# Optimization experiments

Hardware: AMD Instinct MI355X
Metric: run time of the kernel (lower is better)

## Reference

```python
import jax, jax.numpy as jnp
import numpy as np

GROUP = 16
LORA_SCALE = 4.0  # lora_alpha(4*r)/r
EPS = 1e-5


def _dequant(q, scale):
    # q: [O, I] int codes in [0,15]; scale: [O, I//GROUP] per-group normalization
    O, I = q.shape
    s = jnp.repeat(scale, GROUP, axis=1)  # [O, I]
    return (q.astype(jnp.float32) / 15.0 * 2.0 - 1.0) * s


def setup_inputs() -> dict:
    key = jax.random.key(0)
    ks = jax.random.split(key, 6)
    B, D, L, R = 16384, 1024, 18, 32
    x = jax.random.normal(ks[0], (B, D), dtype=jnp.float32)
    q_weights = jax.random.randint(ks[1], (L, D, D), 0, 16, dtype=jnp.int32)
    scales = jax.random.uniform(ks[2], (L, D, D // GROUP), dtype=jnp.float32) * 0.05 + 0.005
    biases = jax.random.normal(ks[3], (L, D), dtype=jnp.float32) * 0.02
    lora_a = jax.random.normal(ks[4], (L, R, D), dtype=jnp.float32) * 0.02
    lora_b = jax.random.normal(ks[5], (L, D, R), dtype=jnp.float32) * 0.02
    ln_gamma = jnp.ones((5, D), dtype=jnp.float32)
    ln_beta = jnp.zeros((5, D), dtype=jnp.float32)
    return {"x": x, "q_weights": q_weights, "scales": scales, "biases": biases,
            "lora_a": lora_a, "lora_b": lora_b, "ln_gamma": ln_gamma, "ln_beta": ln_beta}


def _qlora_linear(x, q, scale, bias, la, lb):
    w = _dequant(q, scale)                       # [O, I]
    base = x @ w.T + bias                        # [B, O]
    lora = (x @ la.T) @ lb.T                     # [B, r] -> [B, O]
    return base + LORA_SCALE * lora


def _layernorm(x, g, b):
    mu = jnp.mean(x, axis=-1, keepdims=True)
    var = jnp.mean(jnp.square(x - mu), axis=-1, keepdims=True)
    return (x - mu) * jax.lax.rsqrt(var + EPS) * g + b


def reference(x, q_weights, scales, biases, lora_a, lora_b, ln_gamma, ln_beta):
    h = x
    for blk in range(6):
        r = h
        for j in range(3):
            li = 3 * blk + j
            r = _qlora_linear(r, q_weights[li], scales[li], biases[li], lora_a[li], lora_b[li])
            if j < 2:
                r = jax.nn.relu(r)
        h = r + h  # residual
        if blk < 5:
            h = _layernorm(h, ln_gamma[blk], ln_beta[blk])
    return h
```

## Files before the change

kernel.cpp:

```cpp
#include <hip/hip_runtime.h>
#include <cstdint>
#include <cstddef>

#define D 1024
#define BATCH 16384
#define NLAYERS 18
#define RR 32

typedef __attribute__((ext_vector_type(8))) __bf16 bf16x8;
typedef __attribute__((ext_vector_type(4))) float f32x4;
typedef __attribute__((address_space(3))) void lds_void_t;
typedef __attribute__((address_space(1))) void gmem_void_t;

union bfpack { unsigned short us[8]; int4 v; };

__device__ __forceinline__ unsigned short f2bf(float f) {
    unsigned int b = __builtin_bit_cast(unsigned int, f);
    b += 0x7fffu + ((b >> 16) & 1u);
    return (unsigned short)(b >> 16);
}
__device__ __forceinline__ float bf2f(unsigned short u) {
    return __builtin_bit_cast(float, (unsigned int)u << 16);
}

__global__ __launch_bounds__(256) void lora_dequant(
    const float* __restrict__ la, const float* __restrict__ lb,
    const int* __restrict__ q, const float* __restrict__ scales,
    unsigned short* __restrict__ weff) {
    __shared__ unsigned short lbs[64][40];
    __shared__ unsigned short lat[256][40];
    __shared__ unsigned short out_s[64][264];
    const int b = blockIdx.x;
    const int li = b >> 6;
    const int o0 = ((b >> 2) & 15) << 6;
    const int i0 = (b & 3) << 8;
    const int t = threadIdx.x;

    {
        const int row = t >> 2, qt = t & 3;
        const float* src = lb + ((size_t)(li * D) + o0 + row) * RR + qt * 8;
        float4 v0 = ((const float4*)src)[0], v1 = ((const float4*)src)[1];
        bfpack u;
        u.us[0] = f2bf(v0.x); u.us[1] = f2bf(v0.y); u.us[2] = f2bf(v0.z); u.us[3] = f2bf(v0.w);
        u.us[4] = f2bf(v1.x); u.us[5] = f2bf(v1.y); u.us[6] = f2bf(v1.z); u.us[7] = f2bf(v1.w);
        *(int4*)&lbs[row][qt * 8] = u.v;
    }
    {
        const int col = t;
#pragma unroll 8
        for (int r = 0; r < 32; ++r)
            lat[col][r] = f2bf(la[((size_t)li * RR + r) * D + i0 + col]);
    }
    __syncthreads();

    {
        const int wid = t >> 6, lane = t & 63;
        const int l15 = lane & 15, kgrp = lane >> 4;
        const int wrow = (wid >> 1) << 5;
        const int wcol = (wid & 1) << 7;
        bf16x8 a[2], bb[8];
#pragma unroll
        for (int f = 0; f < 2; ++f)
            a[f] = *(const bf16x8*)&lbs[wrow + (f << 4) + l15][kgrp << 3];
#pragma unroll
        for (int g = 0; g < 8; ++g)
            bb[g] = *(const bf16x8*)&lat[wcol + (g << 4) + l15][kgrp << 3];
        f32x4 acc[2][8];
#pragma unroll
        for (int i = 0; i < 2; ++i)
#pragma unroll
            for (int j = 0; j < 8; ++j) acc[i][j] = 0.0f;
#pragma unroll
        for (int mi = 0; mi < 2; ++mi)
#pragma unroll
            for (int ni = 0; ni < 8; ++ni)
                acc[mi][ni] = __builtin_amdgcn_mfma_f32_16x16x32_bf16(
                    a[mi], bb[ni], acc[mi][ni], 0, 0, 0);
#pragma unroll
        for (int mi = 0; mi < 2; ++mi) {
            const int row = wrow + (mi << 4) + (kgrp << 2);
#pragma unroll
            for (int ni = 0; ni < 8; ++ni) {
                const int col = wcol + (ni << 4) + l15;
#pragma unroll
                for (int r = 0; r < 4; ++r)
                    out_s[row + r][col] = f2bf(4.0f * acc[mi][ni][r]);
            }
        }
    }
    __syncthreads();

    const float c = 2.0f / 15.0f;
#pragma unroll 1
    for (int iter = 0; iter < 8; ++iter) {
        const int idx = (iter << 8) + t;
        const int row = idx >> 5, c8 = (idx & 31) << 3;
        const size_t grow = (size_t)li * D + o0 + row;
        const int col = i0 + c8;
        const float s = scales[grow * (D / 16) + (col >> 4)];
        const int* qp = q + grow * D + col;
        int4 q0 = ((const int4*)qp)[0], q1 = ((const int4*)qp)[1];
        bfpack lo;
        lo.v = *(const int4*)&out_s[row][c8];
        int qa[8] = {q0.x, q0.y, q0.z, q0.w, q1.x, q1.y, q1.z, q1.w};
        bfpack u;
#pragma unroll
        for (int j = 0; j < 8; ++j)
            u.us[j] = f2bf(((float)qa[j] * c - 1.0f) * s + bf2f(lo.us[j]));
        *(int4*)(weff + grow * D + col) = u.v;
    }
}

__global__ __launch_bounds__(256) void init_xb(const float* __restrict__ x,
                                               unsigned short* __restrict__ xb) {
    const size_t i = (size_t)blockIdx.x * 256 + threadIdx.x;
    float4 v = ((const float4*)x)[i];
    ushort4 u;
    u.x = f2bf(v.x); u.y = f2bf(v.y); u.z = f2bf(v.z); u.w = f2bf(v.w);
    ((ushort4*)xb)[i] = u;
}

#define SBAR() do { asm volatile("" ::: "memory"); __builtin_amdgcn_s_barrier(); asm volatile("" ::: "memory"); } while (0)

__global__ __launch_bounds__(512, 2) void gemm256(
    const unsigned short* __restrict__ xb, const unsigned short* __restrict__ w,
    const float* __restrict__ bias,
    unsigned short* __restrict__ outb, int mode) {
    __shared__ __align__(16) char smem[131072];
    const int tid = threadIdx.x;
    const int wid = tid >> 6, lane = tid & 63;
    const int bid = blockIdx.x + (blockIdx.y << 2);
    const int xcd = bid & 7, slot = bid >> 3;
    const int m0 = ((xcd << 3) + (slot >> 2)) << 8;
    const int n0 = (slot & 3) << 8;
    const int l15 = lane & 15, kgrp = lane >> 4;
    const int wrow = (wid >> 2) << 7;
    const int wcol = (wid & 3) << 6;

    f32x4 acc[8][4];
#pragma unroll
    for (int i = 0; i < 8; ++i)
#pragma unroll
        for (int j = 0; j < 4; ++j) acc[i][j] = 0.0f;

#define STAGE_HALF(hs, i_)                                                     \
    do {                                                                       \
        const int k0_ = (hs) << 5;                                             \
        char* sA_ = smem + ((hs) & 3) * 32768;                                 \
        const int off_ = (i_) * 8192 + (tid << 4);                             \
        const int r_ = off_ >> 6;                                              \
        const int j_ = ((off_ >> 4) & 3) ^ ((r_ >> 1) & 3);                    \
        const unsigned short* ga_ = xb + (size_t)(m0 + r_) * D + k0_ + (j_ << 3); \
        const unsigned short* gb_ = w + (size_t)(n0 + r_) * D + k0_ + (j_ << 3);  \
        char* lA_ = sA_ + (i_) * 8192 + (wid << 10);                           \
        __builtin_amdgcn_global_load_lds((const gmem_void_t*)ga_, (lds_void_t*)lA_, 16, 0, 0);          \
        __builtin_amdgcn_global_load_lds((const gmem_void_t*)gb_, (lds_void_t*)(lA_ + 16384), 16, 0, 0); \
    } while (0)

    STAGE_HALF(0, 0); STAGE_HALF(0, 1);
    STAGE_HALF(1, 0); STAGE_HALF(1, 1);
    STAGE_HALF(2, 0); STAGE_HALF(2, 1);
    asm volatile("s_waitcnt vmcnt(8)" ::: "memory");
    SBAR();

    for (int h = 0; h < 32; ++h) {
        const char* sA = smem + (h & 3) * 32768;
        const char* sB = sA + 16384;
        bf16x8 a[8], b[4];
#pragma unroll
        for (int f = 0; f < 4; ++f) {
            const int r = wrow + (f << 4) + l15;
            a[f] = *(const bf16x8*)(sA + (r << 6) + ((kgrp ^ ((r >> 1) & 3)) << 4));
        }
#pragma unroll
        for (int g = 0; g < 4; ++g) {
            const int r = wcol + (g << 4) + l15;
            b[g] = *(const bf16x8*)(sB + (r << 6) + ((kgrp ^ ((r >> 1) & 3)) << 4));
        }
        if (h < 29) STAGE_HALF(h + 3, 0);
        SBAR();
        asm volatile("s_waitcnt lgkmcnt(0)" ::: "memory");
        __builtin_amdgcn_s_setprio(1);
#pragma unroll
        for (int mi = 0; mi < 4; ++mi)
#pragma unroll
            for (int ni = 0; ni < 4; ++ni)
                acc[mi][ni] = __builtin_amdgcn_mfma_f32_16x16x32_bf16(
                    a[mi], b[ni], acc[mi][ni], 0, 0, 0);
        __builtin_amdgcn_s_setprio(0);
        SBAR();
#pragma unroll
        for (int f = 4; f < 8; ++f) {
            const int r = wrow + (f << 4) + l15;
            a[f] = *(const bf16x8*)(sA + (r << 6) + ((kgrp ^ ((r >> 1) & 3)) << 4));
        }
        if (h < 29) {
            STAGE_HALF(h + 3, 1);
            asm volatile("s_waitcnt vmcnt(8)" ::: "memory");
        } else if (h == 29) {
            asm volatile("s_waitcnt vmcnt(4)" ::: "memory");
        } else if (h == 30) {
            asm volatile("s_waitcnt vmcnt(0)" ::: "memory");
        }
        SBAR();
        asm volatile("s_waitcnt lgkmcnt(0)" ::: "memory");
        __builtin_amdgcn_s_setprio(1);
#pragma unroll
        for (int mi = 4; mi < 8; ++mi)
#pragma unroll
            for (int ni = 0; ni < 4; ++ni)
                acc[mi][ni] = __builtin_amdgcn_mfma_f32_16x16x32_bf16(
                    a[mi], b[ni], acc[mi][ni], 0, 0, 0);
        __builtin_amdgcn_s_setprio(0);
        SBAR();
    }

    const int crow = kgrp << 2;
    float bv[4];
#pragma unroll
    for (int ni = 0; ni < 4; ++ni) bv[ni] = bias[n0 + wcol + (ni << 4) + l15];
#pragma unroll
    for (int mi = 0; mi < 8; ++mi) {
        const int rbase = m0 + wrow + (mi << 4) + crow;
#pragma unroll
        for (int ni = 0; ni < 4; ++ni) {
            const int col = n0 + wcol + (ni << 4) + l15;
#pragma unroll
            for (int r = 0; r < 4; ++r) {
                float v = acc[mi][ni][r] + bv[ni];
                if (mode == 0) v = v > 0.0f ? v : 0.0f;
                outb[(size_t)(rbase + r) * D + col] = f2bf(v);
            }
        }
    }
}

__global__ __launch_bounds__(256) void resid_ln_b(
    unsigned short* __restrict__ hb, const unsigned short* __restrict__ vb,
    const float* __restrict__ gamma, const float* __restrict__ beta) {
    const int row = blockIdx.x;
    const int t = threadIdx.x;
    unsigned short* hr = hb + (size_t)row * D;
    ushort4 hv = ((const ushort4*)hr)[t];
    ushort4 vv = ((const ushort4*)(vb + (size_t)row * D))[t];
    float4 v;
    v.x = bf2f(hv.x) + bf2f(vv.x); v.y = bf2f(hv.y) + bf2f(vv.y);
    v.z = bf2f(hv.z) + bf2f(vv.z); v.w = bf2f(hv.w) + bf2f(vv.w);
    float s = v.x + v.y + v.z + v.w;
    float s2 = v.x * v.x + v.y * v.y + v.z * v.z + v.w * v.w;
#pragma unroll
    for (int off = 32; off > 0; off >>= 1) {
        s += __shfl_down(s, off);
        s2 += __shfl_down(s2, off);
    }
    __shared__ float red[8];
    const int wid = t >> 6, lane = t & 63;
    if (lane == 0) { red[wid] = s; red[wid + 4] = s2; }
    __syncthreads();
    s = red[0] + red[1] + red[2] + red[3];
    s2 = red[4] + red[5] + red[6] + red[7];
    const float mu = s * (1.0f / D);
    const float var = s2 * (1.0f / D) - mu * mu;
    const float rs = rsqrtf(var + 1e-5f);
    float4 g = ((const float4*)gamma)[t];
    float4 b = ((const float4*)beta)[t];
    ushort4 u;
    u.x = f2bf((v.x - mu) * rs * g.x + b.x);
    u.y = f2bf((v.y - mu) * rs * g.y + b.y);
    u.z = f2bf((v.z - mu) * rs * g.z + b.z);
    u.w = f2bf((v.w - mu) * rs * g.w + b.w);
    ((ushort4*)hr)[t] = u;
}

__global__ __launch_bounds__(256) void final_add(
    const unsigned short* __restrict__ hb, const unsigned short* __restrict__ vb,
    float* __restrict__ out) {
    const size_t i = (size_t)blockIdx.x * 256 + threadIdx.x;
    ushort4 hv = ((const ushort4*)hb)[i];
    ushort4 vv = ((const ushort4*)vb)[i];
    float4 o;
    o.x = bf2f(hv.x) + bf2f(vv.x); o.y = bf2f(hv.y) + bf2f(vv.y);
    o.z = bf2f(hv.z) + bf2f(vv.z); o.w = bf2f(hv.w) + bf2f(vv.w);
    ((float4*)out)[i] = o;
}

extern "C" void kernel_launch(void* const* d_in, const int* in_sizes, int n_in,
                              void* d_out, int out_size, void* d_ws, size_t ws_size,
                              hipStream_t stream) {
    const float* x      = (const float*)d_in[0];
    const int*   q      = (const int*)d_in[1];
    const float* scales = (const float*)d_in[2];
    const float* biases = (const float*)d_in[3];
    const float* la     = (const float*)d_in[4];
    const float* lb     = (const float*)d_in[5];
    const float* lng    = (const float*)d_in[6];
    const float* lnb    = (const float*)d_in[7];
    float* out = (float*)d_out;

    char* p = (char*)d_ws;
    unsigned short* weff = (unsigned short*)p; p += (size_t)NLAYERS * D * D * 2;
    unsigned short* xbA  = (unsigned short*)p; p += (size_t)BATCH * D * 2;
    unsigned short* xbB  = (unsigned short*)p; p += (size_t)BATCH * D * 2;
    unsigned short* xbC  = (unsigned short*)p;

    lora_dequant<<<NLAYERS * 16 * 4, 256, 0, stream>>>(la, lb, q, scales, weff);
    init_xb<<<BATCH * D / 4 / 256, 256, 0, stream>>>(x, xbA);

    dim3 ggrid(D / 256, BATCH / 256);
    for (int blk = 0; blk < 6; ++blk) {
        const int li = 3 * blk;
        gemm256<<<ggrid, 512, 0, stream>>>(xbA, weff + (size_t)li * D * D,
                                           biases + (size_t)li * D, xbB, 0);
        gemm256<<<ggrid, 512, 0, stream>>>(xbB, weff + (size_t)(li + 1) * D * D,
                                           biases + (size_t)(li + 1) * D, xbC, 0);
        gemm256<<<ggrid, 512, 0, stream>>>(xbC, weff + (size_t)(li + 2) * D * D,
                                           biases + (size_t)(li + 2) * D, xbB, 1);
        if (blk < 5)
            resid_ln_b<<<BATCH, 256, 0, stream>>>(xbA, xbB,
                                                  lng + (size_t)blk * D, lnb + (size_t)blk * D);
        else
            final_add<<<BATCH * D / 4 / 256, 256, 0, stream>>>(xbA, xbB, out);
    }
}
```

Baseline: 849.7 us.

## Add 256x128 triple-buffered GEMM variant with XCD-aware tiling for odd layers

Adds a second GEMM kernel that uses 256x128 output tiles, a three-stage LDS ring filled by direct global-to-LDS loads, swizzled LDS layout, and a block index remap that groups M tiles per XCD. The new kernel is used for odd-indexed layers while even layers keep the original kernel. The LoRA dequant kernel now aliases its output staging buffer over the input buffers to cut LDS use. The split dispatch looks like an A/B comparison, and the smaller tile raises operand reload traffic in exchange for more blocks and occupancy.

```diff
diff --git a/kernel.cpp b/kernel.cpp
--- a/kernel.cpp
+++ b/kernel.cpp
@@ -27,9 +27,10 @@
     const float* __restrict__ la, const float* __restrict__ lb,
     const int* __restrict__ q, const float* __restrict__ scales,
     unsigned short* __restrict__ weff) {
-    __shared__ unsigned short lbs[64][40];
-    __shared__ unsigned short lat[256][40];
-    __shared__ unsigned short out_s[64][264];
+    __shared__ __align__(16) char lds[33792];
+    unsigned short (*lbs)[40] = (unsigned short (*)[40])lds;
+    unsigned short (*lat)[40] = (unsigned short (*)[40])(lds + 5120);
+    unsigned short (*out_s)[264] = (unsigned short (*)[264])lds;
     const int b = blockIdx.x;
     const int li = b >> 6;
     const int o0 = ((b >> 2) & 15) << 6;
@@ -53,18 +54,20 @@
     }
     __syncthreads();
 
+    const int wid = t >> 6, lane = t & 63;
+    const int l15 = lane & 15, kgrp = lane >> 4;
+    const int wrow = (wid >> 1) << 5;
+    const int wcol = (wid & 1) << 7;
+    bf16x8 a[2], bb[8];
+#pragma unroll
+    for (int f = 0; f < 2; ++f)
+        a[f] = *(const bf16x8*)&lbs[wrow + (f << 4) + l15][kgrp << 3];
+#pragma unroll
+    for (int g = 0; g < 8; ++g)
+        bb[g] = *(const bf16x8*)&lat[wcol + (g << 4) + l15][kgrp << 3];
+    __syncthreads();
+
     {
-        const int wid = t >> 6, lane = t & 63;
-        const int l15 = lane & 15, kgrp = lane >> 4;
-        const int wrow = (wid >> 1) << 5;
-        const int wcol = (wid & 1) << 7;
-        bf16x8 a[2], bb[8];
-#pragma unroll
-        for (int f = 0; f < 2; ++f)
-            a[f] = *(const bf16x8*)&lbs[wrow + (f << 4) + l15][kgrp << 3];
-#pragma unroll
-        for (int g = 0; g < 8; ++g)
-            bb[g] = *(const bf16x8*)&lat[wcol + (g << 4) + l15][kgrp << 3];
         f32x4 acc[2][8];
 #pragma unroll
         for (int i = 0; i < 2; ++i)
@@ -224,6 +227,107 @@
         const int rbase = m0 + wrow + (mi << 4) + crow;
 #pragma unroll
         for (int ni = 0; ni < 4; ++ni) {
+            const int col = n0 + wcol + (ni << 4) + l15;
+#pragma unroll
+            for (int r = 0; r < 4; ++r) {
+                float v = acc[mi][ni][r] + bv[ni];
+                if (mode == 0) v = v > 0.0f ? v : 0.0f;
+                outb[(size_t)(rbase + r) * D + col] = f2bf(v);
+            }
+        }
+    }
+}
+
+__global__ __launch_bounds__(512, 4) void gemm256_v2(
+    const unsigned short* __restrict__ xb, const unsigned short* __restrict__ w,
+    const float* __restrict__ bias,
+    unsigned short* __restrict__ outb, int mode) {
+    __shared__ __align__(16) char smem[73728];
+    const int tid = threadIdx.x;
+    const int wid = tid >> 6, lane = tid & 63;
+    const int bid = blockIdx.x + (blockIdx.y << 3);
+    const int xcd = bid & 7, slot = bid >> 3;
+    const int m0 = ((xcd << 3) + (slot >> 3)) << 8;
+    const int n0 = (slot & 7) << 7;
+    const int l15 = lane & 15, kgrp = lane >> 4;
+    const int wrow = (wid >> 2) << 7;
+    const int wcol = (wid & 3) << 5;
+
+    f32x4 acc[8][2];
+#pragma unroll
+    for (int i = 0; i < 8; ++i)
+#pragma unroll
+        for (int j = 0; j < 2; ++j) acc[i][j] = 0.0f;
+
+#define STAGE2(hs)                                                             \
+    do {                                                                       \
+        const int k0_ = (hs) << 5;                                             \
+        char* b_ = smem + ((hs) % 3) * 24576;                                  \
+        _Pragma("unroll")                                                      \
+        for (int i_ = 0; i_ < 2; ++i_) {                                       \
+            const int off_ = i_ * 8192 + (tid << 4);                           \
+            const int r_ = off_ >> 6;                                          \
+            const int j_ = ((off_ >> 4) & 3) ^ ((r_ >> 1) & 3);                \
+            const unsigned short* ga_ = xb + (size_t)(m0 + r_) * D + k0_ + (j_ << 3); \
+            __builtin_amdgcn_global_load_lds((const gmem_void_t*)ga_,          \
+                (lds_void_t*)(b_ + i_ * 8192 + (wid << 10)), 16, 0, 0);        \
+        }                                                                      \
+        {                                                                      \
+            const int off_ = tid << 4;                                         \
+            const int r_ = off_ >> 6;                                          \
+            const int j_ = ((off_ >> 4) & 3) ^ ((r_ >> 1) & 3);                \
+            const unsigned short* gb_ = w + (size_t)(n0 + r_) * D + k0_ + (j_ << 3);  \
+            __builtin_amdgcn_global_load_lds((const gmem_void_t*)gb_,          \
+                (lds_void_t*)(b_ + 16384 + (wid << 10)), 16, 0, 0);            \
+        }                                                                      \
+    } while (0)
+
+    STAGE2(0); STAGE2(1);
+    asm volatile("s_waitcnt vmcnt(3)" ::: "memory");
+    SBAR();
+
+    for (int h = 0; h < 32; ++h) {
+        const char* sA = smem + (h % 3) * 24576;
+        const char* sB = sA + 16384;
+        bf16x8 a[8], b[2];
+#pragma unroll
+        for (int f = 0; f < 8; ++f) {
+            const int r = wrow + (f << 4) + l15;
+            a[f] = *(const bf16x8*)(sA + (r << 6) + ((kgrp ^ ((r >> 1) & 3)) << 4));
+        }
+#pragma unroll
+        for (int g = 0; g < 2; ++g) {
+            const int r = wcol + (g << 4) + l15;
+            b[g] = *(const bf16x8*)(sB + (r << 6) + ((kgrp ^ ((r >> 1) & 3)) << 4));
+        }
+        if (h < 30) {
+            STAGE2(h + 2);
+            asm volatile("s_waitcnt vmcnt(3)" ::: "memory");
+        } else if (h == 30) {
+            asm volatile("s_waitcnt vmcnt(0)" ::: "memory");
+        }
+        SBAR();
+        asm volatile("s_waitcnt lgkmcnt(0)" ::: "memory");
+        __builtin_amdgcn_s_setprio(1);
+#pragma unroll
+        for (int mi = 0; mi < 8; ++mi)
+#pragma unroll
+            for (int ni = 0; ni < 2; ++ni)
+                acc[mi][ni] = __builtin_amdgcn_mfma_f32_16x16x32_bf16(
+                    a[mi], b[ni], acc[mi][ni], 0, 0, 0);
+        __builtin_amdgcn_s_setprio(0);
+        SBAR();
+    }
+
+    const int crow = kgrp << 2;
+    float bv[2];
+#pragma unroll
+    for (int ni = 0; ni < 2; ++ni) bv[ni] = bias[n0 + wcol + (ni << 4) + l15];
+#pragma unroll
+    for (int mi = 0; mi < 8; ++mi) {
+        const int rbase = m0 + wrow + (mi << 4) + crow;
+#pragma unroll
+        for (int ni = 0; ni < 2; ++ni) {
             const int col = n0 + wcol + (ni << 4) + l15;
 #pragma unroll
             for (int r = 0; r < 4; ++r) {
@@ -284,6 +388,18 @@
     ((float4*)out)[i] = o;
 }
 
+static void run_gemm(const unsigned short* in, const unsigned short* wl,
+                     const float* bias, unsigned short* outb, int mode,
+                     int li, hipStream_t stream) {
+    if (li & 1) {
+        dim3 g(8, 64);
+        gemm256_v2<<<g, 512, 0, stream>>>(in, wl, bias, outb, mode);
+    } else {
+        dim3 g(4, 64);
+        gemm256<<<g, 512, 0, stream>>>(in, wl, bias, outb, mode);
+    }
+}
+
 extern "C" void kernel_launch(void* const* d_in, const int* in_sizes, int n_in,
                               void* d_out, int out_size, void* d_ws, size_t ws_size,
                               hipStream_t stream) {
@@ -306,15 +422,11 @@
     lora_dequant<<<NLAYERS * 16 * 4, 256, 0, stream>>>(la, lb, q, scales, weff);
     init_xb<<<BATCH * D / 4 / 256, 256, 0, stream>>>(x, xbA);
 
-    dim3 ggrid(D / 256, BATCH / 256);
     for (int blk = 0; blk < 6; ++blk) {
         const int li = 3 * blk;
-        gemm256<<<ggrid, 512, 0, stream>>>(xbA, weff + (size_t)li * D * D,
-                                           biases + (size_t)li * D, xbB, 0);
-        gemm256<<<ggrid, 512, 0, stream>>>(xbB, weff + (size_t)(li + 1) * D * D,
-                                           biases + (size_t)(li + 1) * D, xbC, 0);
-        gemm256<<<ggrid, 512, 0, stream>>>(xbC, weff + (size_t)(li + 2) * D * D,
-                                           biases + (size_t)(li + 2) * D, xbB, 1);
+        run_gemm(xbA, weff + (size_t)li * D * D, biases + (size_t)li * D, xbB, 0, li, stream);
+        run_gemm(xbB, weff + (size_t)(li + 1) * D * D, biases + (size_t)(li + 1) * D, xbC, 0, li + 1, stream);
+        run_gemm(xbC, weff + (size_t)(li + 2) * D * D, biases + (size_t)(li + 2) * D, xbB, 1, li + 2, stream);
         if (blk < 5)
             resid_ln_b<<<BATCH, 256, 0, stream>>>(xbA, xbB,
                                                   lng + (size_t)blk * D, lnb + (size_t)blk * D);
```

Result: no change. 863.6 us (+1.6%).
